# Performance work log

Hardware: AMD Instinct MI355X
Metric: run time of the kernel (lower is better)

Reference implementation:

```python
import jax, jax.numpy as jnp
import numpy as np

A_ANCH = 9
NUM_CLASSES = 20


def generate_anchors(anc, grid):
    # anc: (A,2) (w,h); grid: (B,H,W,2) centers -> (B,A,H,W,4) corners
    half = 0.5 * anc  # (A,2)
    c = grid[:, None, :, :, :]                    # (B,1,H,W,2)
    tl = c - half[None, :, None, None, :]         # (B,A,H,W,2)
    br = c + half[None, :, None, None, :]
    return jnp.concatenate([tl, br], axis=-1)


def generate_proposal_yolo(anchors, offsets):
    # anchors, offsets: (B,A,H,W,4); YOLO transform
    w = anchors[..., 2] - anchors[..., 0]
    h = anchors[..., 3] - anchors[..., 1]
    xc = anchors[..., 0] + 0.5 * w + offsets[..., 0]
    yc = anchors[..., 1] + 0.5 * h + offsets[..., 1]
    w = w * jnp.exp(offsets[..., 2])
    h = h * jnp.exp(offsets[..., 3])
    return jnp.stack([xc - 0.5 * w, yc - 0.5 * h, xc + 0.5 * w, yc + 0.5 * h], axis=-1)


def iou(proposals, bboxes):
    # proposals: (B,A,H,W,4); bboxes: (B,N,5) -> (B, A*H*W, N)
    B = proposals.shape[0]
    p = proposals.reshape(B, -1, 1, 4)            # (B,AHW,1,4)
    b = bboxes[:, None, :, :4]                    # (B,1,N,4)
    area_p = (p[..., 2] - p[..., 0]) * (p[..., 3] - p[..., 1])
    area_b = (b[..., 2] - b[..., 0]) * (b[..., 3] - b[..., 1])
    dx = jnp.clip(jnp.minimum(b[..., 2], p[..., 2]) - jnp.maximum(b[..., 0], p[..., 0]), 0)
    dy = jnp.clip(jnp.minimum(b[..., 3], p[..., 3]) - jnp.maximum(b[..., 1], p[..., 1]), 0)
    inter = dx * dy
    return inter / (area_p + area_b - inter)


def conv1x1(x, W, b):
    return jnp.einsum('bchw,oc->bohw', x, W) + b[None, :, None, None]


def extract_anchor_data(anchor_data, idx):
    # anchor_data: (B,A,D,H,W) -> gather rows (M,D)
    B, A, D, H, W = anchor_data.shape
    flat = jnp.transpose(anchor_data, (0, 1, 3, 4, 2)).reshape(-1, D)
    return flat[idx]


def extract_class_scores(all_scores, idx, A):
    # all_scores: (B,C,H,W) -> (M,C), scores shared across A anchors
    B, C, H, W = all_scores.shape
    s = jnp.transpose(all_scores, (0, 2, 3, 1))   # (B,H,W,C)
    s = jnp.broadcast_to(s[:, None], (B, A, H, W, C)).reshape(-1, C)
    return s[idx]


def setup_inputs() -> dict:
    key = jax.random.key(0)
    ks = jax.random.split(key, 12)
    B, Cin, H, W = 32, 256, 64, 64
    A, C, M, N = A_ANCH, NUM_CLASSES, 4096, 64
    hidden, out_dim = 128, 5 * A + C
    features = jax.random.normal(ks[0], (B, Cin, H, W), jnp.float32)
    grid = jax.random.uniform(ks[1], (B, H, W, 2), jnp.float32) * 7.0
    anc = jax.random.uniform(ks[2], (A, 2), jnp.float32) + 0.5
    tl = jax.random.uniform(ks[3], (B, N, 2), jnp.float32) * 3.0
    wh = jax.random.uniform(ks[4], (B, N, 2), jnp.float32) * 3.0 + 0.1
    cls = jax.random.uniform(ks[5], (B, N, 1), jnp.float32)
    bboxes = jnp.concatenate([tl, tl + wh, cls], axis=-1)  # positive-area GT boxes
    GT_offsets = jax.random.normal(ks[6], (M, 4), jnp.float32) * 0.1
    GT_conf_scores = jax.random.uniform(ks[7], (M,), jnp.float32)
    W1 = jax.random.normal(ks[8], (hidden, Cin), jnp.float32) * 0.05
    b1 = jnp.zeros((hidden,), jnp.float32)
    W2 = jax.random.normal(ks[9], (out_dim, hidden), jnp.float32) * 0.05
    b2 = jnp.zeros((out_dim,), jnp.float32)
    n_total = B * A * H * W
    pos_anchor_idx = jax.random.randint(ks[10], (M,), 0, n_total, jnp.int64 if jax.config.jax_enable_x64 else jnp.int32)
    neg_anchor_idx = jax.random.randint(ks[11], (M,), 0, n_total, jnp.int64 if jax.config.jax_enable_x64 else jnp.int32)
    return {"features": features, "grid": grid, "anc": anc, "bboxes": bboxes,
            "GT_offsets": GT_offsets, "GT_conf_scores": GT_conf_scores,
            "W1": W1, "b1": b1, "W2": W2, "b2": b2,
            "pos_anchor_idx": pos_anchor_idx, "neg_anchor_idx": neg_anchor_idx}


def reference(features, grid, anc, bboxes, GT_offsets, GT_conf_scores,
              W1, b1, W2, b2, pos_anchor_idx, neg_anchor_idx):
    B = features.shape[0]
    A = A_ANCH
    H, W = features.shape[2], features.shape[3]
    # PredictionNetwork (eval mode: dropout is identity)
    hdn = jax.nn.leaky_relu(conv1x1(features, W1, b1))  # LeakyReLU slope 0.01
    out = conv1x1(hdn, W2, b2)                           # (B,5A+C,H,W)
    conf_all = out[:, :A]                                # (B,A,H,W)
    off_all = out[:, A:5 * A].reshape(B, A, 4, H, W)
    off_all = off_all.at[:, :, :2].set(jax.nn.sigmoid(off_all[:, :, :2]) - 0.5)
    cls_all = out[:, 5 * A:]                             # (B,C,H,W)
    # training-mode extraction
    conf_pos = extract_anchor_data(conf_all[:, :, None], pos_anchor_idx)  # (M,1)
    conf_neg = extract_anchor_data(conf_all[:, :, None], neg_anchor_idx)
    conf_scores = jax.nn.sigmoid(jnp.concatenate([conf_pos, conf_neg], axis=0))  # (2M,1)
    offsets_pos = extract_anchor_data(off_all, pos_anchor_idx)            # (M,4)
    class_scores = extract_class_scores(cls_all, pos_anchor_idx, A)       # (M,C)
    # anchors -> proposals -> IoU
    anchors = generate_anchors(anc, grid)                                 # (B,A,H,W,4)
    proposals = generate_proposal_yolo(anchors, jnp.transpose(off_all, (0, 1, 3, 4, 2)))
    iou_mat = iou(anchors, bboxes)                                        # (B,AHW,N)
    # SSE losses (YOLO-style)
    gt_conf = jnp.concatenate([jnp.ones_like(GT_conf_scores),
                               jnp.zeros_like(GT_conf_scores)], axis=0).reshape(-1, 1)
    conf_loss = jnp.sum((conf_scores - gt_conf) ** 2) / gt_conf.shape[0]
    reg_loss = jnp.sum((offsets_pos - GT_offsets) ** 2) / GT_offsets.shape[0]
    return proposals, iou_mat, conf_loss, reg_loss, class_scores
```

## Files before the change

### kernel.cpp

```cpp
#include <hip/hip_runtime.h>
#include <math.h>

typedef __attribute__((ext_vector_type(8))) short short8;
typedef __attribute__((ext_vector_type(4))) float f32x4;

#define HW    4096
#define B_    32
#define CIN   256
#define HID   128
#define A_    9
#define NCLS  20
#define M_    4096
#define NBOX  64
#define S_TOT (B_*HW)

#define PROP_SIZE (B_*A_*HW*4)
#define IOU_OFF   ((size_t)PROP_SIZE)
#define IOU_SIZE  ((size_t)B_*A_*HW*NBOX)
#define CONF_LOSS_OFF (IOU_OFF + IOU_SIZE)
#define REG_LOSS_OFF  (CONF_LOSS_OFF + 1)
#define CLS_OFF       (CONF_LOSS_OFF + 2)

#define WS_W1A_F 0
#define WS_W2A_F 16384
#define WS_B2P   21504
#define WS_CONF  21632
#define WS_OFF4  (WS_CONF + B_*A_*HW)
#define WS_CLS   (WS_OFF4 + B_*A_*HW*4)

__device__ __forceinline__ unsigned short f2bf(float x) {
    unsigned int u = __float_as_uint(x);
    unsigned int r = (u + 0x7FFFu + ((u >> 16) & 1u)) >> 16;
    return (unsigned short)r;
}
__device__ __forceinline__ float vrcp(float x) {
    float r; asm("v_rcp_f32 %0, %1" : "=v"(r) : "v"(x)); return r;
}
__device__ __forceinline__ float vexp2(float x) {
    float r; asm("v_exp_f32 %0, %1" : "=v"(r) : "v"(x)); return r;
}
__device__ __forceinline__ float fexp(float x)  { return vexp2(x * 1.44269504f); }
__device__ __forceinline__ float fsig(float x)  { return vrcp(1.0f + fexp(-x)); }

__device__ __forceinline__ int fbt_addr(int col, int k) {
    return col * 512 + ((k * 2) ^ ((col & 31) << 4));
}
__device__ __forceinline__ int hbt_addr(int col, int k) {
    return col * 256 + ((k * 2) ^ ((col & 7) << 4));
}

__global__ __launch_bounds__(256) void prep_weights(
    const float* __restrict__ W1, const float* __restrict__ W2,
    const float* __restrict__ b2, float* __restrict__ ws)
{
    int t = blockIdx.x * 256 + threadIdx.x;
    unsigned short* W1a = (unsigned short*)(ws + WS_W1A_F);
    unsigned short* W2a = (unsigned short*)(ws + WS_W2A_F);
    if (t < 32768) {
        int j = t & 7, l = (t >> 3) & 63, f = t >> 9;
        int ks = f >> 3, m = f & 7;
        int row = m * 16 + (l & 15);
        int k   = ks * 32 + (l >> 4) * 8 + j;
        W1a[t] = f2bf(W1[row * CIN + k]);
    } else if (t < 32768 + 10240) {
        int u = t - 32768;
        int j = u & 7, l = (u >> 3) & 63, f = u >> 9;
        int ks = f / 5, m = f % 5;
        int row = m * 16 + (l & 15);
        int k   = ks * 32 + (l >> 4) * 8 + j;
        W2a[u] = f2bf(row < 65 ? W2[row * HID + k] : 0.0f);
    } else if (t < 32768 + 10240 + 80) {
        int v = t - 43008;
        ws[WS_B2P + v] = (v < 65) ? b2[v] : 0.0f;
    }
}

__global__ __launch_bounds__(256, 4) void conv_mfma(
    const float* __restrict__ features, const float* __restrict__ grid,
    const float* __restrict__ anc,      const float* __restrict__ b1,
    const float* __restrict__ bboxes,
    float* __restrict__ ws,             float* __restrict__ dout)
{
    __shared__ __align__(16) char smem[32768];

    const int tid = threadIdx.x;
    const int s0  = blockIdx.x * 64;
    const int b   = s0 >> 12;
    const int hw0 = s0 & (HW - 1);
    const int col = tid & 63;
    const int wv  = tid >> 6;
    const int ln  = tid & 63;
    const int kg  = ln >> 4;
    const int colg = wv * 16 + (ln & 15);

    {
        const int g = ln >> 4, q = ln & 15;
        const float* fb = features + (size_t)b * CIN * HW + hw0;
        #pragma unroll
        for (int i = 0; i < 16; ++i) {
            const int k = i * 16 + wv * 4 + g;
            const float4 v = *(const float4*)(fb + (size_t)k * HW + 4 * q);
            float t0 = __shfl_xor(v.x, 32), t1 = __shfl_xor(v.y, 32);
            float t2 = __shfl_xor(v.z, 32), t3 = __shfl_xor(v.w, 32);
            const bool h2 = (g & 2) != 0;
            float p0 = h2 ? t2 : v.x, p1 = h2 ? t3 : v.y;
            float p2 = h2 ? v.z : t0, p3 = h2 ? v.w : t1;
            float u0 = __shfl_xor(p0, 16), u1 = __shfl_xor(p1, 16);
            float u2 = __shfl_xor(p2, 16), u3 = __shfl_xor(p3, 16);
            const bool h1 = (g & 1) != 0;
            float c0 = h1 ? u1 : p0, c1 = h1 ? p1 : u0;
            float c2 = h1 ? u3 : p2, c3 = h1 ? p3 : u2;
            const int k0 = i * 16 + wv * 4;
            uint2 pk;
            pk.x = (unsigned)f2bf(c0) | ((unsigned)f2bf(c1) << 16);
            pk.y = (unsigned)f2bf(c2) | ((unsigned)f2bf(c3) << 16);
            *(uint2*)(smem + fbt_addr(4 * q + g, k0)) = pk;
        }
    }
    __syncthreads();

    const unsigned short* W1a = (const unsigned short*)(ws + WS_W1A_F);
    f32x4 acc[8];
    #pragma unroll
    for (int m = 0; m < 8; ++m) acc[m] = (f32x4){0.f, 0.f, 0.f, 0.f};
    #pragma unroll
    for (int ks = 0; ks < 8; ++ks) {
        short8 bf = *(const short8*)(smem + fbt_addr(colg, ks * 32 + kg * 8));
        #pragma unroll
        for (int m = 0; m < 8; ++m) {
            short8 af = *(const short8*)(W1a + ((ks * 8 + m) * 64 + ln) * 8);
            acc[m] = __builtin_amdgcn_mfma_f32_16x16x32_bf16(af, bf, acc[m], 0, 0, 0);
        }
    }
    __syncthreads();

    #pragma unroll
    for (int m = 0; m < 8; ++m) {
        float4 bv = *(const float4*)(b1 + m * 16 + kg * 4);
        float v0 = acc[m][0] + bv.x, v1 = acc[m][1] + bv.y;
        float v2 = acc[m][2] + bv.z, v3 = acc[m][3] + bv.w;
        v0 = v0 > 0.f ? v0 : 0.01f * v0;  v1 = v1 > 0.f ? v1 : 0.01f * v1;
        v2 = v2 > 0.f ? v2 : 0.01f * v2;  v3 = v3 > 0.f ? v3 : 0.01f * v3;
        unsigned int lo = (unsigned int)f2bf(v0) | ((unsigned int)f2bf(v1) << 16);
        unsigned int hi = (unsigned int)f2bf(v2) | ((unsigned int)f2bf(v3) << 16);
        *(uint2*)(smem + hbt_addr(colg, m * 16 + kg * 4)) = make_uint2(lo, hi);
    }
    __syncthreads();

    const unsigned short* W2a = (const unsigned short*)(ws + WS_W2A_F);
    f32x4 a2[5];
    #pragma unroll
    for (int m = 0; m < 5; ++m) a2[m] = (f32x4){0.f, 0.f, 0.f, 0.f};
    #pragma unroll
    for (int ks = 0; ks < 4; ++ks) {
        short8 bf = *(const short8*)(smem + hbt_addr(colg, ks * 32 + kg * 8));
        #pragma unroll
        for (int m = 0; m < 5; ++m) {
            short8 af = *(const short8*)(W2a + ((ks * 5 + m) * 64 + ln) * 8);
            a2[m] = __builtin_amdgcn_mfma_f32_16x16x32_bf16(af, bf, a2[m], 0, 0, 0);
        }
    }

    {
        const int hwi = ln >> 4;
        const int nq  = ln & 15;
        float bx0[4], by0[4], bx2[4], by2[4], areab[4];
        #pragma unroll
        for (int j = 0; j < 4; ++j) {
            const float* bb = bboxes + ((size_t)b * NBOX + nq * 4 + j) * 5;
            bx0[j] = bb[0]; by0[j] = bb[1]; bx2[j] = bb[2]; by2[j] = bb[3];
            areab[j] = (bx2[j] - bx0[j]) * (by2[j] - by0[j]);
        }
        const float2* gp = (const float2*)grid + (size_t)b * HW;
        float* ioub = dout + IOU_OFF + (size_t)b * A_ * HW * NBOX;
        for (int t = 0; t < 4; ++t) {
            int hw = hw0 + wv * 16 + t * 4 + hwi;
            float2 g = gp[hw];
            float e2x[4], e0x[4], e2y[4], e0y[4];
            #pragma unroll
            for (int j = 0; j < 4; ++j) {
                e2x[j] = bx2[j] - g.x;  e0x[j] = bx0[j] - g.x;
                e2y[j] = by2[j] - g.y;  e0y[j] = by0[j] - g.y;
            }
            #pragma unroll
            for (int a = 0; a < A_; ++a) {
                float hwd = 0.5f * anc[2 * a], hh = 0.5f * anc[2 * a + 1];
                float ap  = 4.0f * hwd * hh;
                f32x4 res;
                #pragma unroll
                for (int j = 0; j < 4; ++j) {
                    float dx = fmaxf(fminf(e2x[j], hwd) - fmaxf(e0x[j], -hwd), 0.0f);
                    float dy = fmaxf(fminf(e2y[j], hh ) - fmaxf(e0y[j], -hh ), 0.0f);
                    float inter = dx * dy;
                    res[j] = inter * vrcp(ap + areab[j] - inter);
                }
                __builtin_nontemporal_store(
                    res, (f32x4*)(ioub + ((size_t)a * HW + hw) * NBOX + nq * 4));
            }
        }
    }
    __syncthreads();

    float* Ot = (float*)smem;
    const float* b2p = ws + WS_B2P;
    #pragma unroll
    for (int m = 0; m < 5; ++m) {
        float4 bv = *(const float4*)(b2p + m * 16 + kg * 4);
        #pragma unroll
        for (int i = 0; i < 4; ++i)
            Ot[(m * 16 + kg * 4 + i) * 65 + colg] = a2[m][i] + ((const float*)&bv)[i];
    }
    __syncthreads();

    const float* OtC = (const float*)smem;
    const int hw = hw0 + col;
    if (wv == 0) {
        #pragma unroll
        for (int a = 0; a < A_; ++a)
            ws[WS_CONF + (size_t)(b * A_ + a) * HW + hw] = OtC[a * 65 + col];
    } else if (wv == 3) {
        #pragma unroll
        for (int c = 0; c < NCLS; ++c)
            ws[WS_CLS + (size_t)c * S_TOT + b * HW + hw] = OtC[(45 + c) * 65 + col];
    } else {
        const float2 g2 = ((const float2*)grid)[(size_t)b * HW + hw];
        int a0 = (wv == 1) ? 0 : 4;
        int a1 = (wv == 1) ? 4 : 9;
        for (int a = a0; a < a1; ++a) {
            float t0 = OtC[(A_ + 4 * a + 0) * 65 + col];
            float t1 = OtC[(A_ + 4 * a + 1) * 65 + col];
            float t2 = OtC[(A_ + 4 * a + 2) * 65 + col];
            float t3 = OtC[(A_ + 4 * a + 3) * 65 + col];
            t0 = fsig(t0) - 0.5f;
            t1 = fsig(t1) - 0.5f;
            size_t idx = (size_t)(b * A_ + a) * HW + hw;
            ((float4*)(ws + WS_OFF4))[idx] = make_float4(t0, t1, t2, t3);
            float aw = anc[2 * a], ah = anc[2 * a + 1];
            float xc = g2.x + t0, yc = g2.y + t1;
            float wn = aw * fexp(t2), hn = ah * fexp(t3);
            f32x4 prop = {xc - 0.5f * wn, yc - 0.5f * hn,
                          xc + 0.5f * wn, yc + 0.5f * hn};
            __builtin_nontemporal_store(prop, (f32x4*)dout + idx);
        }
    }
}

__global__ __launch_bounds__(256) void tail_kernel(
    const float* __restrict__ ws, const float* __restrict__ GT_offsets,
    const int* __restrict__ pos_idx, const int* __restrict__ neg_idx,
    float* __restrict__ dout)
{
    int tid = threadIdx.x;
    if (blockIdx.x < 320) {
        int t = blockIdx.x * 256 + tid;
        int m = t / NCLS, c = t % NCLS;
        int ip = pos_idx[m];
        int bb = ip / (A_ * HW);
        int hw = ip & (HW - 1);
        dout[CLS_OFF + t] = ws[WS_CLS + (size_t)c * S_TOT + bb * HW + hw];
        return;
    }
    float conf_sum = 0.0f, reg_sum = 0.0f;
    for (int m = tid; m < M_; m += 256) {
        int ip = pos_idx[m], in_ = neg_idx[m];
        float cp = fsig(ws[WS_CONF + ip]);
        float cn = fsig(ws[WS_CONF + in_]);
        conf_sum += (cp - 1.0f) * (cp - 1.0f) + cn * cn;
        float4 off = ((const float4*)(ws + WS_OFF4))[ip];
        float d0 = off.x - GT_offsets[4 * m + 0];
        float d1 = off.y - GT_offsets[4 * m + 1];
        float d2 = off.z - GT_offsets[4 * m + 2];
        float d3 = off.w - GT_offsets[4 * m + 3];
        reg_sum += d0 * d0 + d1 * d1 + d2 * d2 + d3 * d3;
    }
    #pragma unroll
    for (int off = 32; off > 0; off >>= 1) {
        conf_sum += __shfl_down(conf_sum, off);
        reg_sum  += __shfl_down(reg_sum, off);
    }
    __shared__ float rc[4], rr[4];
    int w = tid >> 6;
    if ((tid & 63) == 0) { rc[w] = conf_sum; rr[w] = reg_sum; }
    __syncthreads();
    if (tid == 0) {
        float c = rc[0] + rc[1] + rc[2] + rc[3];
        float r = rr[0] + rr[1] + rr[2] + rr[3];
        dout[CONF_LOSS_OFF] = c / (2.0f * M_);
        dout[REG_LOSS_OFF]  = r / (float)M_;
    }
}

extern "C" void kernel_launch(void* const* d_in, const int* in_sizes, int n_in,
                              void* d_out, int out_size, void* d_ws, size_t ws_size,
                              hipStream_t stream) {
    const float* features    = (const float*)d_in[0];
    const float* grid        = (const float*)d_in[1];
    const float* anc         = (const float*)d_in[2];
    const float* bboxes      = (const float*)d_in[3];
    const float* GT_offsets  = (const float*)d_in[4];
    const float* W1          = (const float*)d_in[6];
    const float* b1          = (const float*)d_in[7];
    const float* W2          = (const float*)d_in[8];
    const float* b2          = (const float*)d_in[9];
    const int*   pos_idx     = (const int*)d_in[10];
    const int*   neg_idx     = (const int*)d_in[11];
    float* out = (float*)d_out;
    float* ws  = (float*)d_ws;

    prep_weights<<<169, 256, 0, stream>>>(W1, W2, b2, ws);
    conv_mfma<<<S_TOT / 64, 256, 0, stream>>>(features, grid, anc, b1, bboxes, ws, out);
    tail_kernel<<<321, 256, 0, stream>>>(ws, GT_offsets, pos_idx, neg_idx, out);
}
```

Before: 118.7 us.

## Split IoU into separate blocks interleaved with conv blocks in one launch

Moves the IoU computation out of the conv/MFMA blocks into dedicated IoU blocks. Conv and IoU blocks are interleaved within a single grid so compute-heavy conv work overlaps with the store-bound IoU writes. Each IoU wave handles one (batch, anchor, 128-position) slice, giving long contiguous store streams. The cost is that the grid values are loaded twice, and IoU blocks still reserve the kernel's shared memory and launch bounds.

```diff
diff --git a/kernel.cpp b/kernel.cpp
--- a/kernel.cpp
+++ b/kernel.cpp
@@ -27,6 +27,10 @@
 #define WS_CONF  21632
 #define WS_OFF4  (WS_CONF + B_*A_*HW)
 #define WS_CLS   (WS_OFF4 + B_*A_*HW*4)
+
+#define NCONV 2048
+#define NIOU  2304
+#define NBLK  (NCONV + NIOU)
 
 __device__ __forceinline__ unsigned short f2bf(float x) {
     unsigned int u = __float_as_uint(x);
@@ -75,21 +79,65 @@
     }
 }
 
-__global__ __launch_bounds__(256, 4) void conv_mfma(
+__global__ __launch_bounds__(256, 4) void fused_kernel(
     const float* __restrict__ features, const float* __restrict__ grid,
     const float* __restrict__ anc,      const float* __restrict__ b1,
     const float* __restrict__ bboxes,
     float* __restrict__ ws,             float* __restrict__ dout)
 {
+    const int bid = blockIdx.x;
+    const int tid = threadIdx.x;
+    const int wv  = tid >> 6;
+    const int ln  = tid & 63;
+
+    bool is_conv; int idx;
+    if (bid < 2 * NCONV) { is_conv = (bid & 1) == 0; idx = bid >> 1; }
+    else                 { is_conv = false;          idx = NCONV + (bid - 2 * NCONV); }
+
+    if (!is_conv) {
+        const int cid = idx * 4 + wv;
+        const int b   = cid / (A_ * 32);
+        const int rem = cid % (A_ * 32);
+        const int a   = rem / 32;
+        const int hw0 = (rem % 32) * 128;
+        const int hwi = ln >> 4;
+        const int nq  = ln & 15;
+
+        float bx0[4], by0[4], bx2[4], by2[4], areab[4];
+        #pragma unroll
+        for (int j = 0; j < 4; ++j) {
+            const float* bb = bboxes + ((size_t)b * NBOX + nq * 4 + j) * 5;
+            bx0[j] = bb[0]; by0[j] = bb[1]; bx2[j] = bb[2]; by2[j] = bb[3];
+            areab[j] = (bx2[j] - bx0[j]) * (by2[j] - by0[j]);
+        }
+        const float hwd = 0.5f * anc[2 * a], hh = 0.5f * anc[2 * a + 1];
+        const float ap  = 4.0f * hwd * hh;
+        const float2* gp = (const float2*)grid + (size_t)b * HW;
+        float* ioub = dout + IOU_OFF + (size_t)(b * A_ + a) * HW * NBOX;
+        #pragma unroll 4
+        for (int t = 0; t < 32; ++t) {
+            const int hw = hw0 + t * 4 + hwi;
+            const float2 g = gp[hw];
+            f32x4 res;
+            #pragma unroll
+            for (int j = 0; j < 4; ++j) {
+                float dx = fmaxf(fminf(bx2[j] - g.x, hwd) - fmaxf(bx0[j] - g.x, -hwd), 0.0f);
+                float dy = fmaxf(fminf(by2[j] - g.y, hh ) - fmaxf(by0[j] - g.y, -hh ), 0.0f);
+                float inter = dx * dy;
+                res[j] = inter * vrcp(ap + areab[j] - inter);
+            }
+            __builtin_nontemporal_store(
+                res, (f32x4*)(ioub + ((size_t)hw) * NBOX + nq * 4));
+        }
+        return;
+    }
+
     __shared__ __align__(16) char smem[32768];
 
-    const int tid = threadIdx.x;
-    const int s0  = blockIdx.x * 64;
+    const int s0  = idx * 64;
     const int b   = s0 >> 12;
     const int hw0 = s0 & (HW - 1);
     const int col = tid & 63;
-    const int wv  = tid >> 6;
-    const int ln  = tid & 63;
     const int kg  = ln >> 4;
     const int colg = wv * 16 + (ln & 15);
 
@@ -160,45 +208,6 @@
             a2[m] = __builtin_amdgcn_mfma_f32_16x16x32_bf16(af, bf, a2[m], 0, 0, 0);
         }
     }
-
-    {
-        const int hwi = ln >> 4;
-        const int nq  = ln & 15;
-        float bx0[4], by0[4], bx2[4], by2[4], areab[4];
-        #pragma unroll
-        for (int j = 0; j < 4; ++j) {
-            const float* bb = bboxes + ((size_t)b * NBOX + nq * 4 + j) * 5;
-            bx0[j] = bb[0]; by0[j] = bb[1]; bx2[j] = bb[2]; by2[j] = bb[3];
-            areab[j] = (bx2[j] - bx0[j]) * (by2[j] - by0[j]);
-        }
-        const float2* gp = (const float2*)grid + (size_t)b * HW;
-        float* ioub = dout + IOU_OFF + (size_t)b * A_ * HW * NBOX;
-        for (int t = 0; t < 4; ++t) {
-            int hw = hw0 + wv * 16 + t * 4 + hwi;
-            float2 g = gp[hw];
-            float e2x[4], e0x[4], e2y[4], e0y[4];
-            #pragma unroll
-            for (int j = 0; j < 4; ++j) {
-                e2x[j] = bx2[j] - g.x;  e0x[j] = bx0[j] - g.x;
-                e2y[j] = by2[j] - g.y;  e0y[j] = by0[j] - g.y;
-            }
-            #pragma unroll
-            for (int a = 0; a < A_; ++a) {
-                float hwd = 0.5f * anc[2 * a], hh = 0.5f * anc[2 * a + 1];
-                float ap  = 4.0f * hwd * hh;
-                f32x4 res;
-                #pragma unroll
-                for (int j = 0; j < 4; ++j) {
-                    float dx = fmaxf(fminf(e2x[j], hwd) - fmaxf(e0x[j], -hwd), 0.0f);
-                    float dy = fmaxf(fminf(e2y[j], hh ) - fmaxf(e0y[j], -hh ), 0.0f);
-                    float inter = dx * dy;
-                    res[j] = inter * vrcp(ap + areab[j] - inter);
-                }
-                __builtin_nontemporal_store(
-                    res, (f32x4*)(ioub + ((size_t)a * HW + hw) * NBOX + nq * 4));
-            }
-        }
-    }
     __syncthreads();
 
     float* Ot = (float*)smem;
@@ -233,14 +242,14 @@
             float t3 = OtC[(A_ + 4 * a + 3) * 65 + col];
             t0 = fsig(t0) - 0.5f;
             t1 = fsig(t1) - 0.5f;
-            size_t idx = (size_t)(b * A_ + a) * HW + hw;
-            ((float4*)(ws + WS_OFF4))[idx] = make_float4(t0, t1, t2, t3);
+            size_t odx = (size_t)(b * A_ + a) * HW + hw;
+            ((float4*)(ws + WS_OFF4))[odx] = make_float4(t0, t1, t2, t3);
             float aw = anc[2 * a], ah = anc[2 * a + 1];
             float xc = g2.x + t0, yc = g2.y + t1;
             float wn = aw * fexp(t2), hn = ah * fexp(t3);
             f32x4 prop = {xc - 0.5f * wn, yc - 0.5f * hn,
                           xc + 0.5f * wn, yc + 0.5f * hn};
-            __builtin_nontemporal_store(prop, (f32x4*)dout + idx);
+            __builtin_nontemporal_store(prop, (f32x4*)dout + odx);
         }
     }
 }
@@ -308,6 +317,6 @@
     float* ws  = (float*)d_ws;
 
     prep_weights<<<169, 256, 0, stream>>>(W1, W2, b2, ws);
-    conv_mfma<<<S_TOT / 64, 256, 0, stream>>>(features, grid, anc, b1, bboxes, ws, out);
+    fused_kernel<<<NBLK, 256, 0, stream>>>(features, grid, anc, b1, bboxes, ws, out);
     tail_kernel<<<321, 256, 0, stream>>>(ws, GT_offsets, pos_idx, neg_idx, out);
 }
```

After: 108.6 us. -8.5%, faster.
